# Kernel tuning notes

Measured on AMD Instinct MI355X. Metric: run time of the kernel, lower is better.

Reference implementation:

```python
import jax, jax.numpy as jnp
import numpy as np

N_NODES = 100000
NEG_SLOPE = 0.01  # torch F.leaky_relu default


def sage_gcn_layer(feat, src, dst, W, b):
    # DGL SAGEConv, aggregator_type='gcn':
    #   h_i = fc_neigh((sum_{j->i} x_j + x_i) / (in_deg_i + 1))
    neigh_sum = jax.ops.segment_sum(feat[src], dst, num_segments=N_NODES)
    deg = jax.ops.segment_sum(jnp.ones((src.shape[0],), feat.dtype), dst,
                              num_segments=N_NODES)
    h = (neigh_sum + feat) / (deg + 1.0)[:, None]
    return h @ W + b


def setup_inputs() -> dict:
    key = jax.random.key(0)
    k_feat, k_e, k_w1, k_w2 = jax.random.split(key, 4)
    d_in, d_hid, d_out = 128, 128, 128
    E = 1600000
    feat = jax.random.normal(k_feat, (N_NODES, d_in), dtype=jnp.float32)
    edge_index = jax.random.randint(k_e, (2, E), 0, N_NODES, dtype=jnp.int64)
    W1 = jax.random.normal(k_w1, (d_in, d_hid), dtype=jnp.float32) / np.sqrt(d_in)
    b1 = jnp.zeros((d_hid,), jnp.float32)
    W2 = jax.random.normal(k_w2, (d_hid, d_out), dtype=jnp.float32) / np.sqrt(d_hid)
    b2 = jnp.zeros((d_out,), jnp.float32)
    return {"feat": feat, "edge_index": edge_index,
            "W1": W1, "b1": b1, "W2": W2, "b2": b2}


def reference(feat, edge_index, W1, b1, W2, b2):
    src, dst = edge_index[0], edge_index[1]
    h = sage_gcn_layer(feat, src, dst, W1, b1)
    h = jax.nn.leaky_relu(h, NEG_SLOPE)
    # dropout = 0 -> identity
    h = sage_gcn_layer(h, src, dst, W2, b2)
    return jax.nn.leaky_relu(h, NEG_SLOPE)
```

## Files before the change

kernel.cpp:

```cpp
#include <hip/hip_runtime.h>

#define NEG_SLOPE 0.01f
#define BSHIFT 8
#define BMASK 255
#define BMAX 512
#define CAPB 5120
#define SCCH 6144

typedef __attribute__((ext_vector_type(8))) short bf16x8;
typedef __attribute__((ext_vector_type(4))) float f32x4;
typedef __attribute__((ext_vector_type(2))) float f32x2;
typedef __attribute__((ext_vector_type(4))) unsigned u32x4;

static __device__ inline unsigned short f2b(float f) {
    unsigned u = __builtin_bit_cast(unsigned, f);
    return (unsigned short)((u + 0x7FFF + ((u >> 16) & 1)) >> 16);
}
static __device__ inline float b2f_lo(unsigned u) {
    return __builtin_bit_cast(float, u << 16);
}
static __device__ inline float b2f_hi(unsigned u) {
    return __builtin_bit_cast(float, u & 0xFFFF0000u);
}

__global__ __launch_bounds__(256) void front_kernel(const float* __restrict__ W1,
                                                    const float* __restrict__ W2,
                                                    unsigned short* __restrict__ Wt1,
                                                    unsigned short* __restrict__ Wt2,
                                                    int* __restrict__ bcursor) {
    int i = blockIdx.x * 256 + threadIdx.x;
    if (i < BMAX) bcursor[i] = 0;
    int n = i & 127, k = i >> 7;
    Wt1[n * 128 + k] = f2b(W1[k * 128 + n]);
    Wt2[n * 128 + k] = f2b(W2[k * 128 + n]);
}

__global__ __launch_bounds__(256) void bscatter_kernel(const int* __restrict__ src,
                                                       const int* __restrict__ dst,
                                                       int* __restrict__ bcursor,
                                                       unsigned* __restrict__ pairs,
                                                       int E, int B) {
    __shared__ int h[BMAX];
    __shared__ int base[BMAX];
    __shared__ int dl[SCCH];
    const int t = threadIdx.x;
    for (int i = t; i < B; i += 256) h[i] = 0;
    __syncthreads();
    const int e0 = blockIdx.x * SCCH;
    const int e1 = min(e0 + SCCH, E);
    for (int e = e0 + t; e < e1; e += 256) {
        int d = dst[e];
        dl[e - e0] = d;
        atomicAdd(&h[d >> BSHIFT], 1);
    }
    __syncthreads();
    for (int i = t; i < B; i += 256) {
        int c = h[i];
        base[i] = c ? atomicAdd(&bcursor[i], c) : 0;
    }
    __syncthreads();
    for (int i = t; i < B; i += 256) h[i] = base[i];
    __syncthreads();
    for (int e = e0 + t; e < e1; e += 256) {
        int d = dl[e - e0];
        int bb = d >> BSHIFT;
        int pos = atomicAdd(&h[bb], 1);
        if (pos < CAPB)
            pairs[(size_t)bb * CAPB + pos] = (unsigned)src[e] | ((unsigned)(d & BMASK) << 24);
    }
}

__global__ __launch_bounds__(256) void bfinal_kernel(const unsigned* __restrict__ pairs,
                                                     const int* __restrict__ bcursor,
                                                     int* __restrict__ offsets,
                                                     int* __restrict__ degs,
                                                     int* __restrict__ csr, int N) {
    __shared__ int h[256];
    __shared__ int cur[256];
    const int b = blockIdx.x;
    const int t = threadIdx.x;
    const int cnt = min(bcursor[b], CAPB);
    const unsigned* __restrict__ pb = pairs + (size_t)b * CAPB;
    h[t] = 0;
    __syncthreads();
    for (int e = t; e < cnt; e += 256)
        atomicAdd(&h[pb[e] >> 24], 1);
    __syncthreads();
    int v = h[t];
    for (int d = 1; d < 256; d <<= 1) {
        int u = (t >= d) ? h[t - d] : 0;
        __syncthreads();
        h[t] += u;
        __syncthreads();
    }
    const int prefix = h[t] - v;
    const int node = (b << BSHIFT) + t;
    if (node < N) {
        offsets[node] = b * CAPB + prefix;
        degs[node] = v;
    }
    cur[t] = prefix;
    __syncthreads();
    int* __restrict__ cb = csr + (size_t)b * CAPB;
    for (int e = t; e < cnt; e += 256) {
        unsigned pr = pb[e];
        int pos = atomicAdd(&cur[pr >> 24], 1);
        cb[pos] = (int)(pr & 0xFFFFFFu);
    }
}

template <bool IN_F32>
__global__ __launch_bounds__(256) void gemm_xw(const void* __restrict__ inA,
                                               const unsigned short* __restrict__ Wt,
                                               unsigned short* __restrict__ outy,
                                               int N) {
    __shared__ unsigned short Wa[128 * 128];
    const int tid = threadIdx.x;
    const int row0 = blockIdx.x * 128;

#pragma unroll
    for (int it = 0; it < 8; ++it) {
        int idx = it * 256 + tid;
        int r = idx >> 4, c = idx & 15;
        uint4 v = *(const uint4*)(Wt + r * 128 + c * 8);
        *(uint4*)(Wa + r * 128 + ((c ^ (r & 15)) << 3)) = v;
    }
    __syncthreads();

    const int w = tid >> 6;
    const int lane = tid & 63;
    const int m = lane & 15;
    const int q = lane >> 4;

    const int r0 = row0 + w * 32 + m;
    const size_t ar0 = (size_t)min(r0, N - 1) * 128;
    const size_t ar1 = (size_t)min(r0 + 16, N - 1) * 128;

    f32x4 acc[2][8];
#pragma unroll
    for (int rt = 0; rt < 2; ++rt)
#pragma unroll
        for (int ct = 0; ct < 8; ++ct) acc[rt][ct] = (f32x4){0.f, 0.f, 0.f, 0.f};

#pragma unroll
    for (int kk = 0; kk < 4; ++kk) {
        const int chunk = kk * 4 + q;
        bf16x8 af0, af1;
        if (IN_F32) {
            const float* Af = (const float*)inA;
            float4 u0 = *(const float4*)(Af + ar0 + chunk * 8);
            float4 u1 = *(const float4*)(Af + ar0 + chunk * 8 + 4);
            float4 u2 = *(const float4*)(Af + ar1 + chunk * 8);
            float4 u3 = *(const float4*)(Af + ar1 + chunk * 8 + 4);
            af0[0] = (short)f2b(u0.x); af0[1] = (short)f2b(u0.y);
            af0[2] = (short)f2b(u0.z); af0[3] = (short)f2b(u0.w);
            af0[4] = (short)f2b(u1.x); af0[5] = (short)f2b(u1.y);
            af0[6] = (short)f2b(u1.z); af0[7] = (short)f2b(u1.w);
            af1[0] = (short)f2b(u2.x); af1[1] = (short)f2b(u2.y);
            af1[2] = (short)f2b(u2.z); af1[3] = (short)f2b(u2.w);
            af1[4] = (short)f2b(u3.x); af1[5] = (short)f2b(u3.y);
            af1[6] = (short)f2b(u3.z); af1[7] = (short)f2b(u3.w);
        } else {
            const unsigned short* Ab = (const unsigned short*)inA;
            af0 = *(const bf16x8*)(Ab + ar0 + chunk * 8);
            af1 = *(const bf16x8*)(Ab + ar1 + chunk * 8);
        }
#pragma unroll
        for (int ct = 0; ct < 8; ++ct) {
            int n = ct * 16 + m;
            bf16x8 bfr = *(const bf16x8*)(Wa + n * 128 + ((chunk ^ (n & 15)) << 3));
            acc[0][ct] = __builtin_amdgcn_mfma_f32_16x16x32_bf16(af0, bfr, acc[0][ct], 0, 0, 0);
            acc[1][ct] = __builtin_amdgcn_mfma_f32_16x16x32_bf16(af1, bfr, acc[1][ct], 0, 0, 0);
        }
    }

#pragma unroll
    for (int ct = 0; ct < 8; ++ct) {
        const int gcol = ct * 16 + m;
#pragma unroll
        for (int rt = 0; rt < 2; ++rt) {
#pragma unroll
            for (int reg = 0; reg < 4; ++reg) {
                int grow = row0 + w * 32 + rt * 16 + q * 4 + reg;
                if (grow < N)
                    outy[(long long)grow * 128 + gcol] = f2b(acc[rt][ct][reg]);
            }
        }
    }
}

static __device__ inline f32x2 up2(unsigned u) {
    return (f32x2){ b2f_lo(u), b2f_hi(u) };
}

#define GATHER(dst, off) \
    asm volatile("global_load_dwordx4 %0, %1, %2" : "=v"(dst) : "v"(off), "s"(xc))
#define ACC4(u) do { A0 += up2((u).x); A1 += up2((u).y); \
                     A2 += up2((u).z); A3 += up2((u).w); } while (0)
#define ACCM(u, mk) do { \
    A0 += up2((u).x & (mk)); A1 += up2((u).y & (mk)); \
    A2 += up2((u).z & (mk)); A3 += up2((u).w & (mk)); } while (0)

static __device__ __forceinline__ unsigned rowsel(int g, unsigned poff,
                                                  int i0, int i1, int i2, int i3) {
    int s01 = (g & 1) ? i1 : i0;
    int s23 = (g & 1) ? i3 : i2;
    int s = (g & 2) ? s23 : s01;
    return ((unsigned)s << 8) | poff;
}

template <bool OUT_F32>
__global__ __launch_bounds__(256) void agg_apply(const unsigned short* __restrict__ xb,
                                                 const int* __restrict__ offsets,
                                                 const int* __restrict__ degs,
                                                 const int* __restrict__ csr,
                                                 const float* __restrict__ bias,
                                                 void* __restrict__ outv, int N) {
    const int node = (blockIdx.x * blockDim.x + threadIdx.x) >> 6;
    if (node >= N) return;
    const int lane = threadIdx.x & 63;
    const int g = lane >> 4;
    const unsigned poff = (unsigned)((lane & 15) << 4);
    const char* __restrict__ xc = (const char*)xb;

    const int nu = __builtin_amdgcn_readfirstlane(node);
    const int start = __builtin_amdgcn_readfirstlane(offsets[nu]);
    const int deg   = __builtin_amdgcn_readfirstlane(degs[nu]);
    const int rounds = deg >> 2;
    const int tailn  = deg & 3;

    u32x4 vs = (u32x4){0, 0, 0, 0};
    if (g == 0) GATHER(vs, ((unsigned)nu << 8) | poff);

    f32x2 A0 = {0.f, 0.f}, A1 = {0.f, 0.f}, A2 = {0.f, 0.f}, A3 = {0.f, 0.f};

    int r = 0;
    while (r + 4 <= rounds) {
        const int p = start + (r << 2);
        int i0  = csr[p +  0], i1  = csr[p +  1], i2  = csr[p +  2], i3  = csr[p +  3];
        int i4  = csr[p +  4], i5  = csr[p +  5], i6  = csr[p +  6], i7  = csr[p +  7];
        int i8  = csr[p +  8], i9  = csr[p +  9], i10 = csr[p + 10], i11 = csr[p + 11];
        int i12 = csr[p + 12], i13 = csr[p + 13], i14 = csr[p + 14], i15 = csr[p + 15];
        unsigned a0 = rowsel(g, poff, i0,  i1,  i2,  i3);
        unsigned a1 = rowsel(g, poff, i4,  i5,  i6,  i7);
        unsigned a2 = rowsel(g, poff, i8,  i9,  i10, i11);
        unsigned a3 = rowsel(g, poff, i12, i13, i14, i15);
        __builtin_amdgcn_sched_barrier(0);
        u32x4 v0, v1, v2, v3;
        GATHER(v0, a0); GATHER(v1, a1); GATHER(v2, a2); GATHER(v3, a3);
        asm volatile("s_waitcnt vmcnt(0)" ::: "memory");
        __builtin_amdgcn_sched_barrier(0);
        ACC4(v0); ACC4(v1); ACC4(v2); ACC4(v3);
        r += 4;
    }

    const int rr = rounds - r;
    const int p = start + (r << 2);
    u32x4 v0, v1, v2, vt;
    if (rr >= 1) {
        int i0 = csr[p + 0], i1 = csr[p + 1], i2 = csr[p + 2], i3 = csr[p + 3];
        GATHER(v0, rowsel(g, poff, i0, i1, i2, i3));
    }
    if (rr >= 2) {
        int i0 = csr[p + 4], i1 = csr[p + 5], i2 = csr[p + 6], i3 = csr[p + 7];
        GATHER(v1, rowsel(g, poff, i0, i1, i2, i3));
    }
    if (rr >= 3) {
        int i0 = csr[p + 8], i1 = csr[p + 9], i2 = csr[p + 10], i3 = csr[p + 11];
        GATHER(v2, rowsel(g, poff, i0, i1, i2, i3));
    }
    const unsigned mt = (g < tailn) ? ~0u : 0u;
    if (tailn) {
        const int q = start + (rounds << 2);
        int t0 = csr[q];
        int t1 = (tailn > 1) ? csr[q + 1] : t0;
        int t2 = (tailn > 2) ? csr[q + 2] : t0;
        GATHER(vt, rowsel(g, poff, t0, t1, t2, t0));
    }
    asm volatile("s_waitcnt vmcnt(0)" ::: "memory");
    __builtin_amdgcn_sched_barrier(0);
    if (rr >= 1) ACC4(v0);
    if (rr >= 2) ACC4(v1);
    if (rr >= 3) ACC4(v2);
    if (tailn) ACCM(vt, mt);

    float a[8];
    a[0] = A0.x; a[1] = A0.y; a[2] = A1.x; a[3] = A1.y;
    a[4] = A2.x; a[5] = A2.y; a[6] = A3.x; a[7] = A3.y;
#pragma unroll
    for (int i = 0; i < 8; ++i) {
        a[i] += __shfl_xor(a[i], 16);
        a[i] += __shfl_xor(a[i], 32);
    }
    a[0] += b2f_lo(vs.x); a[1] += b2f_hi(vs.x);
    a[2] += b2f_lo(vs.y); a[3] += b2f_hi(vs.y);
    a[4] += b2f_lo(vs.z); a[5] += b2f_hi(vs.z);
    a[6] += b2f_lo(vs.w); a[7] += b2f_hi(vs.w);

    const float inv = 1.0f / (float)(deg + 1);
    if (g == 0) {
        const int c0 = (lane & 15) << 3;
        const float4 bb0 = *(const float4*)(bias + c0);
        const float4 bb1 = *(const float4*)(bias + c0 + 4);
        float rv[8];
        rv[0] = a[0] * inv + bb0.x; rv[1] = a[1] * inv + bb0.y;
        rv[2] = a[2] * inv + bb0.z; rv[3] = a[3] * inv + bb0.w;
        rv[4] = a[4] * inv + bb1.x; rv[5] = a[5] * inv + bb1.y;
        rv[6] = a[6] * inv + bb1.z; rv[7] = a[7] * inv + bb1.w;
#pragma unroll
        for (int k = 0; k < 8; ++k) rv[k] = rv[k] > 0.f ? rv[k] : rv[k] * NEG_SLOPE;
        if (OUT_F32) {
            float* op = (float*)outv + (size_t)node * 128 + c0;
            *(float4*)op = make_float4(rv[0], rv[1], rv[2], rv[3]);
            *(float4*)(op + 4) = make_float4(rv[4], rv[5], rv[6], rv[7]);
        } else {
            uint4 o;
            o.x = (unsigned)f2b(rv[0]) | ((unsigned)f2b(rv[1]) << 16);
            o.y = (unsigned)f2b(rv[2]) | ((unsigned)f2b(rv[3]) << 16);
            o.z = (unsigned)f2b(rv[4]) | ((unsigned)f2b(rv[5]) << 16);
            o.w = (unsigned)f2b(rv[6]) | ((unsigned)f2b(rv[7]) << 16);
            *(uint4*)((char*)outv + (((unsigned)node << 8) | poff)) = o;
        }
    }
}

extern "C" void kernel_launch(void* const* d_in, const int* in_sizes, int n_in,
                              void* d_out, int out_size, void* d_ws, size_t ws_size,
                              hipStream_t stream) {
    const float* feat = (const float*)d_in[0];
    const int*   edges = (const int*)d_in[1];
    const float* W1 = (const float*)d_in[2];
    const float* b1 = (const float*)d_in[3];
    const float* W2 = (const float*)d_in[4];
    const float* b2 = (const float*)d_in[5];
    float* out = (float*)d_out;

    const int N = in_sizes[0] / 128;
    const int E = in_sizes[1] / 2;
    const int* src = edges;
    const int* dst = edges + E;
    const int B = (N + (1 << BSHIFT) - 1) >> BSHIFT;

    unsigned short* T1  = (unsigned short*)d_ws;
    unsigned short* T2  = T1 + (size_t)N * 128;
    unsigned*       pairs = (unsigned*)T2;
    unsigned short* Wt1 = T2 + (size_t)N * 128;
    unsigned short* Wt2 = Wt1 + 128 * 128;
    int* offsets = (int*)(Wt2 + 128 * 128);
    int* degs    = offsets + ((N + 8) & ~7);
    int* bcursor = degs + ((N + 8) & ~7);
    int* csr     = bcursor + 512;

    const int gemmGrid = (N + 127) / 128;
    const int aggGrid  = (N + 3) / 4;
    const int scGrid   = (E + SCCH - 1) / SCCH;

    front_kernel<<<64, 256, 0, stream>>>(W1, W2, Wt1, Wt2, bcursor);
    gemm_xw<true><<<gemmGrid, 256, 0, stream>>>(feat, Wt1, T1, N);
    bscatter_kernel<<<scGrid, 256, 0, stream>>>(src, dst, bcursor, pairs, E, B);
    bfinal_kernel<<<B, 256, 0, stream>>>(pairs, bcursor, offsets, degs, csr, N);
    agg_apply<false><<<aggGrid, 256, 0, stream>>>(T1, offsets, degs, csr, b1,
                                                  (void*)T2, N);
    gemm_xw<false><<<gemmGrid, 256, 0, stream>>>(T2, Wt2, T1, N);
    agg_apply<true><<<aggGrid, 256, 0, stream>>>(T1, offsets, degs, csr, b2,
                                                 (void*)out, N);
}
```

Baseline: 299.1 us.

## Fold weight transpose into bucket scatter and stage bucket sort in LDS

The weight transpose/bf16 conversion moves into extra blocks of the scatter kernel, and the cursor reset becomes a memset, which removes one kernel launch. The scatter kernel now uses 1024-thread blocks with 4096-edge chunks and vectorized int4 loads of src/dst kept in registers instead of an LDS copy. The bucket finalize kernel stages each bucket in LDS, sorts it locally and writes the CSR contiguously instead of scattering to global memory. The trade-off is larger shared memory use per block, which lowers occupancy, and the memset adds an extra API call.

Result: faster. 277.7 us (-7.1%).

```diff
diff --git a/kernel.cpp b/kernel.cpp
--- a/kernel.cpp
+++ b/kernel.cpp
@@ -5,7 +5,7 @@
 #define BMASK 255
 #define BMAX 512
 #define CAPB 5120
-#define SCCH 6144
+#define SCCH 4096
 
 typedef __attribute__((ext_vector_type(8))) short bf16x8;
 typedef __attribute__((ext_vector_type(4))) float f32x4;
@@ -23,90 +23,109 @@
     return __builtin_bit_cast(float, u & 0xFFFF0000u);
 }
 
-__global__ __launch_bounds__(256) void front_kernel(const float* __restrict__ W1,
-                                                    const float* __restrict__ W2,
-                                                    unsigned short* __restrict__ Wt1,
-                                                    unsigned short* __restrict__ Wt2,
-                                                    int* __restrict__ bcursor) {
-    int i = blockIdx.x * 256 + threadIdx.x;
-    if (i < BMAX) bcursor[i] = 0;
-    int n = i & 127, k = i >> 7;
-    Wt1[n * 128 + k] = f2b(W1[k * 128 + n]);
-    Wt2[n * 128 + k] = f2b(W2[k * 128 + n]);
-}
-
-__global__ __launch_bounds__(256) void bscatter_kernel(const int* __restrict__ src,
-                                                       const int* __restrict__ dst,
-                                                       int* __restrict__ bcursor,
-                                                       unsigned* __restrict__ pairs,
-                                                       int E, int B) {
+__global__ __launch_bounds__(1024) void bscatter_kernel(const int* __restrict__ src,
+                                                        const int* __restrict__ dst,
+                                                        int* __restrict__ bcursor,
+                                                        unsigned* __restrict__ pairs,
+                                                        const float* __restrict__ W1,
+                                                        const float* __restrict__ W2,
+                                                        unsigned short* __restrict__ Wt1,
+                                                        unsigned short* __restrict__ Wt2,
+                                                        int E, int B, int scGrid) {
+    const int bx = blockIdx.x;
+    const int t = threadIdx.x;
+    if (bx >= scGrid) {
+        int i = (bx - scGrid) * 1024 + t;
+        int n = i & 127, k = i >> 7;
+        Wt1[n * 128 + k] = f2b(W1[k * 128 + n]);
+        Wt2[n * 128 + k] = f2b(W2[k * 128 + n]);
+        return;
+    }
     __shared__ int h[BMAX];
     __shared__ int base[BMAX];
-    __shared__ int dl[SCCH];
-    const int t = threadIdx.x;
-    for (int i = t; i < B; i += 256) h[i] = 0;
-    __syncthreads();
-    const int e0 = blockIdx.x * SCCH;
+    for (int i = t; i < B; i += 1024) h[i] = 0;
+    __syncthreads();
+    const int e0 = bx * SCCH;
     const int e1 = min(e0 + SCCH, E);
-    for (int e = e0 + t; e < e1; e += 256) {
-        int d = dst[e];
-        dl[e - e0] = d;
-        atomicAdd(&h[d >> BSHIFT], 1);
-    }
-    __syncthreads();
-    for (int i = t; i < B; i += 256) {
+    const int idx = e0 + t * 4;
+    const int nv = min(max(e1 - idx, 0), 4);
+    int d0 = 0, d1 = 0, d2 = 0, d3 = 0, s0 = 0, s1 = 0, s2 = 0, s3 = 0;
+    if (nv == 4) {
+        int4 d4 = *(const int4*)(dst + idx);
+        int4 s4 = *(const int4*)(src + idx);
+        d0 = d4.x; d1 = d4.y; d2 = d4.z; d3 = d4.w;
+        s0 = s4.x; s1 = s4.y; s2 = s4.z; s3 = s4.w;
+    } else if (nv > 0) {
+        d0 = dst[idx]; s0 = src[idx];
+        if (nv > 1) { d1 = dst[idx + 1]; s1 = src[idx + 1]; }
+        if (nv > 2) { d2 = dst[idx + 2]; s2 = src[idx + 2]; }
+    }
+    if (nv > 0) atomicAdd(&h[d0 >> BSHIFT], 1);
+    if (nv > 1) atomicAdd(&h[d1 >> BSHIFT], 1);
+    if (nv > 2) atomicAdd(&h[d2 >> BSHIFT], 1);
+    if (nv > 3) atomicAdd(&h[d3 >> BSHIFT], 1);
+    __syncthreads();
+    for (int i = t; i < B; i += 1024) {
         int c = h[i];
         base[i] = c ? atomicAdd(&bcursor[i], c) : 0;
     }
     __syncthreads();
-    for (int i = t; i < B; i += 256) h[i] = base[i];
-    __syncthreads();
-    for (int e = e0 + t; e < e1; e += 256) {
-        int d = dl[e - e0];
-        int bb = d >> BSHIFT;
-        int pos = atomicAdd(&h[bb], 1);
-        if (pos < CAPB)
-            pairs[(size_t)bb * CAPB + pos] = (unsigned)src[e] | ((unsigned)(d & BMASK) << 24);
-    }
-}
-
-__global__ __launch_bounds__(256) void bfinal_kernel(const unsigned* __restrict__ pairs,
-                                                     const int* __restrict__ bcursor,
-                                                     int* __restrict__ offsets,
-                                                     int* __restrict__ degs,
-                                                     int* __restrict__ csr, int N) {
+    for (int i = t; i < B; i += 1024) h[i] = base[i];
+    __syncthreads();
+#define SCAT(dd, ss) do { int bb = (dd) >> BSHIFT; int pos = atomicAdd(&h[bb], 1); \
+    if (pos < CAPB) pairs[(size_t)bb * CAPB + pos] = \
+        (unsigned)(ss) | ((unsigned)((dd) & BMASK) << 24); } while (0)
+    if (nv > 0) SCAT(d0, s0);
+    if (nv > 1) SCAT(d1, s1);
+    if (nv > 2) SCAT(d2, s2);
+    if (nv > 3) SCAT(d3, s3);
+#undef SCAT
+}
+
+__global__ __launch_bounds__(1024) void bfinal_kernel(const unsigned* __restrict__ pairs,
+                                                      const int* __restrict__ bcursor,
+                                                      int* __restrict__ offsets,
+                                                      int* __restrict__ degs,
+                                                      int* __restrict__ csr, int N) {
+    __shared__ unsigned stage[CAPB];
+    __shared__ unsigned sorted[CAPB];
     __shared__ int h[256];
     __shared__ int cur[256];
     const int b = blockIdx.x;
     const int t = threadIdx.x;
     const int cnt = min(bcursor[b], CAPB);
     const unsigned* __restrict__ pb = pairs + (size_t)b * CAPB;
-    h[t] = 0;
-    __syncthreads();
-    for (int e = t; e < cnt; e += 256)
-        atomicAdd(&h[pb[e] >> 24], 1);
-    __syncthreads();
-    int v = h[t];
+    if (t < 256) h[t] = 0;
+    for (int e = t; e < cnt; e += 1024) stage[e] = pb[e];
+    __syncthreads();
+    for (int e = t; e < cnt; e += 1024)
+        atomicAdd(&h[stage[e] >> 24], 1);
+    __syncthreads();
+    int v = (t < 256) ? h[t] : 0;
     for (int d = 1; d < 256; d <<= 1) {
-        int u = (t >= d) ? h[t - d] : 0;
+        int u = (t < 256 && t >= d) ? h[t - d] : 0;
         __syncthreads();
-        h[t] += u;
+        if (t < 256) h[t] += u;
         __syncthreads();
     }
-    const int prefix = h[t] - v;
-    const int node = (b << BSHIFT) + t;
-    if (node < N) {
-        offsets[node] = b * CAPB + prefix;
-        degs[node] = v;
-    }
-    cur[t] = prefix;
+    if (t < 256) {
+        const int prefix = h[t] - v;
+        const int node = (b << BSHIFT) + t;
+        if (node < N) {
+            offsets[node] = b * CAPB + prefix;
+            degs[node] = v;
+        }
+        cur[t] = prefix;
+    }
+    __syncthreads();
+    for (int e = t; e < cnt; e += 1024) {
+        unsigned pr = stage[e];
+        int pos = atomicAdd(&cur[pr >> 24], 1);
+        sorted[pos] = pr & 0xFFFFFFu;
+    }
     __syncthreads();
     int* __restrict__ cb = csr + (size_t)b * CAPB;
-    for (int e = t; e < cnt; e += 256) {
-        unsigned pr = pb[e];
-        int pos = atomicAdd(&cur[pr >> 24], 1);
-        cb[pos] = (int)(pr & 0xFFFFFFu);
-    }
+    for (int e = t; e < cnt; e += 1024) cb[e] = (int)sorted[e];
 }
 
 template <bool IN_F32>
@@ -355,10 +374,12 @@
     const int aggGrid  = (N + 3) / 4;
     const int scGrid   = (E + SCCH - 1) / SCCH;
 
-    front_kernel<<<64, 256, 0, stream>>>(W1, W2, Wt1, Wt2, bcursor);
+    hipMemsetAsync(bcursor, 0, (size_t)BMAX * sizeof(int), stream);
+    bscatter_kernel<<<scGrid + 16, 1024, 0, stream>>>(src, dst, bcursor, pairs,
+                                                      W1, W2, Wt1, Wt2,
+                                                      E, B, scGrid);
     gemm_xw<true><<<gemmGrid, 256, 0, stream>>>(feat, Wt1, T1, N);
-    bscatter_kernel<<<scGrid, 256, 0, stream>>>(src, dst, bcursor, pairs, E, B);
-    bfinal_kernel<<<B, 256, 0, stream>>>(pairs, bcursor, offsets, degs, csr, N);
+    bfinal_kernel<<<B, 1024, 0, stream>>>(pairs, bcursor, offsets, degs, csr, N);
     agg_apply<false><<<aggGrid, 256, 0, stream>>>(T1, offsets, degs, csr, b1,
                                                   (void*)T2, N);
     gemm_xw<false><<<gemmGrid, 256, 0, stream>>>(T2, Wt2, T1, N);
```
